# Performance work log

Measured on AMD Instinct MI355X. Metric: run time of the kernel, lower is better.

## Reference

```python
import jax, jax.numpy as jnp
import numpy as np

N_NODES = 50000


def gcn_conv(x, src, dst, deg_inv_sqrt, W, b, n_nodes):
    # GCNConv: h = x @ W; msg = norm * h[src]; out = scatter_add(msg, dst) + b
    h = x @ W  # [N, out]
    norm = deg_inv_sqrt[src] * deg_inv_sqrt[dst]  # symmetric normalization
    msg = h[src] * norm[:, None]  # [E+N, out]
    out = jax.ops.segment_sum(msg, dst, num_segments=n_nodes)
    return out + b


def setup_inputs() -> dict:
    key = jax.random.key(0)
    k_x, k_e, k_w1, k_w2 = jax.random.split(key, 4)
    in_c, hid, out_c = 256, 64, 64
    x = jax.random.normal(k_x, (N_NODES, 256), dtype=jnp.float32)
    edge_index = jax.random.randint(k_e, (2, 1600000), 0, N_NODES, dtype=jnp.int64)
    # Glorot-ish weights, zero bias as in GCNConv defaults
    W1 = jax.random.normal(k_w1, (in_c, hid), dtype=jnp.float32) / np.sqrt(in_c)
    b1 = jnp.zeros((hid,), dtype=jnp.float32)
    W2 = jax.random.normal(k_w2, (hid, out_c), dtype=jnp.float32) / np.sqrt(hid)
    b2 = jnp.zeros((out_c,), dtype=jnp.float32)
    return {"x": x, "edge_index": edge_index, "W1": W1, "b1": b1, "W2": W2, "b2": b2}


def reference(x, edge_index, W1, b1, W2, b2):
    n = x.shape[0]
    loops = jnp.arange(n, dtype=edge_index.dtype)
    src = jnp.concatenate([edge_index[0], loops])  # add self-loops
    dst = jnp.concatenate([edge_index[1], loops])
    deg = jax.ops.segment_sum(jnp.ones_like(dst, dtype=x.dtype), dst, num_segments=n)
    deg_inv_sqrt = jnp.where(deg > 0, jax.lax.rsqrt(deg), 0.0)
    h = gcn_conv(x, src, dst, deg_inv_sqrt, W1, b1, n)
    h = jax.nn.relu(h)
    out = gcn_conv(h, src, dst, deg_inv_sqrt, W2, b2, n)
    return out
```

## Files before the change

### kernel.cpp

```cpp
#include <hip/hip_runtime.h>
#include <hip/hip_bf16.h>


#define NB_MAX 1024

__device__ inline unsigned short f2bf(float f) {
    unsigned u = __builtin_bit_cast(unsigned, f);
    return (unsigned short)((u + 0x7FFFu + ((u >> 16) & 1u)) >> 16);
}
__device__ inline float blo(unsigned u) {
    return __builtin_bit_cast(float, u << 16);
}
__device__ inline float bhi(unsigned u) {
    return __builtin_bit_cast(float, u & 0xFFFF0000u);
}


__global__ __launch_bounds__(1024) void k_hist(const int* __restrict__ ei, int E,
                                               int nb, int chunk,
                                               int* __restrict__ histT) {
    __shared__ int h[NB_MAX];
    for (int i = threadIdx.x; i < nb; i += 1024) h[i] = 0;
    __syncthreads();
    int e0 = blockIdx.x * chunk, e1 = min(E, e0 + chunk);
    for (int e = e0 + threadIdx.x; e < e1; e += 1024)
        atomicAdd(&h[ei[E + e] >> 6], 1);
    __syncthreads();
    for (int b = threadIdx.x; b < nb; b += 1024)
        histT[b * 256 + blockIdx.x] = h[b];
}


__global__ __launch_bounds__(256) void k_scan_cols(int* __restrict__ histT,
                                                   int* __restrict__ total) {
    __shared__ int sm[256];
    int b = blockIdx.x, t = threadIdx.x;
    int v = histT[b * 256 + t];
    sm[t] = v;
    __syncthreads();
    for (int off = 1; off < 256; off <<= 1) {
        int u = (t >= off) ? sm[t - off] : 0;
        __syncthreads();
        sm[t] += u;
        __syncthreads();
    }
    histT[b * 256 + t] = sm[t] - v;
    if (t == 255) total[b] = sm[255];
}


__global__ __launch_bounds__(1024) void k_scan_totals(const int* __restrict__ total,
                                                      int* __restrict__ base, int nb) {
    __shared__ int sm[1024];
    int t = threadIdx.x;
    int v = (t < nb) ? total[t] : 0;
    sm[t] = v;
    __syncthreads();
    for (int off = 1; off < 1024; off <<= 1) {
        int u = (t >= off) ? sm[t - off] : 0;
        __syncthreads();
        sm[t] += u;
        __syncthreads();
    }
    if (t < nb) base[t] = sm[t] - v;
    if (t == nb - 1) base[nb] = sm[t];
}


__global__ __launch_bounds__(1024) void k_scatter(const int* __restrict__ ei, int E,
                                                  int nb, int chunk,
                                                  const int* __restrict__ histT,
                                                  const int* __restrict__ base,
                                                  unsigned* __restrict__ packed) {
    __shared__ int cur[NB_MAX];
    for (int b = threadIdx.x; b < nb; b += 1024)
        cur[b] = base[b] + histT[b * 256 + blockIdx.x];
    __syncthreads();
    int e0 = blockIdx.x * chunk, e1 = min(E, e0 + chunk);
    for (int e = e0 + threadIdx.x; e < e1; e += 1024) {
        int s = ei[e], d = ei[E + e];
        int pos = atomicAdd(&cur[d >> 6], 1);
        packed[pos] = (unsigned)s | ((unsigned)(d & 63) << 16);
    }
}


__global__ __launch_bounds__(1024) void k_csr(const unsigned* __restrict__ packed,
                                              const int* __restrict__ base,
                                              int n,
                                              int* __restrict__ qbeg,
                                              int* __restrict__ qcnt,
                                              float* __restrict__ dinv,
                                              unsigned short* __restrict__ ssrcp,
                                              unsigned short* __restrict__ hs1,
                                              unsigned short* __restrict__ hs2) {
    __shared__ int cnt[64];
    __shared__ int cur[64];
    const int b = blockIdx.x, t = threadIdx.x;
    const int p0 = base[b], p1 = base[b + 1];
    if (t < 64) cnt[t] = 0;
    __syncthreads();
    for (int p = p0 + t; p < p1; p += 1024)
        atomicAdd(&cnt[(packed[p] >> 16) & 63], 1);
    __syncthreads();
    if (t < 64) {
        int deg = cnt[t];
        int pdeg = (deg + 1) & ~1;
        int sum = pdeg;
#pragma unroll
        for (int d = 1; d < 64; d <<= 1) {
            int u = __shfl_up(sum, d, 64);
            if (t >= d) sum += u;
        }
        int excl = sum - pdeg;
        int pb = (2 + p0 + 128 * b + 1) & ~1;
        int start = pb + excl;
        int node = (b << 6) + t;
        if (node < n) {
            qbeg[node] = start >> 1;
            qcnt[node] = pdeg >> 1;
            dinv[node] = 1.0f / sqrtf((float)(deg + 1));
        }
        cur[t] = start;
    }
    __syncthreads();
    for (int p = p0 + t; p < p1; p += 1024) {
        unsigned k = packed[p];
        int pos = atomicAdd(&cur[(k >> 16) & 63], 1);
        ssrcp[pos] = (unsigned short)(k & 0xFFFFu);
    }
    __syncthreads();
    if (t < 64 && (cnt[t] & 1))
        ssrcp[cur[t]] = (unsigned short)n;
    if (b == 0) {
        if (t < 64) {
            hs1[(size_t)n * 64 + t] = 0;
            hs2[(size_t)n * 64 + t] = 0;
        }
        if (t == 0) {
            ssrcp[0] = (unsigned short)n;
            ssrcp[1] = (unsigned short)n;
        }
    }
}

#define FMA4(A, s, wv)                                                         \
    (A).x += (s) * (wv).x; (A).y += (s) * (wv).y;                              \
    (A).z += (s) * (wv).z; (A).w += (s) * (wv).w;


__global__ __launch_bounds__(256) void k_gemm256(const float* __restrict__ X,
                                                 const float* __restrict__ W,
                                                 const float* __restrict__ dinv,
                                                 unsigned short* __restrict__ HS,
                                                 int n) {
    const int K = 256;
    __shared__ float xl[128][36];
    __shared__ float wl[32][64];

    const int t = threadIdx.x;
    const int tc = t & 15;
    const int tr = t >> 4;
    const int row0 = blockIdx.x * 128;

    float4 acc[8];
#pragma unroll
    for (int r = 0; r < 8; ++r) acc[r] = make_float4(0.f, 0.f, 0.f, 0.f);

    for (int k0 = 0; k0 < K; k0 += 32) {
#pragma unroll
        for (int i = 0; i < 4; ++i) {
            int idx = i * 256 + t;
            int r = idx >> 3, f4 = idx & 7;
            int gr = row0 + r;
            float4 v = make_float4(0.f, 0.f, 0.f, 0.f);
            if (gr < n) v = *(const float4*)(X + (size_t)gr * K + k0 + f4 * 4);
            *(float4*)&xl[r][f4 * 4] = v;
        }
#pragma unroll
        for (int i = 0; i < 2; ++i) {
            int idx = i * 256 + t;
            int kr = idx >> 4, f4 = idx & 15;
            *(float4*)&wl[kr][f4 * 4] =
                *(const float4*)(W + (size_t)(k0 + kr) * 64 + f4 * 4);
        }
        __syncthreads();

#pragma unroll
        for (int kk = 0; kk < 32; kk += 4) {
            float4 wv0 = *(float4*)&wl[kk + 0][tc * 4];
            float4 wv1 = *(float4*)&wl[kk + 1][tc * 4];
            float4 wv2 = *(float4*)&wl[kk + 2][tc * 4];
            float4 wv3 = *(float4*)&wl[kk + 3][tc * 4];
#pragma unroll
            for (int r = 0; r < 8; ++r) {
                float4 xv = *(float4*)&xl[tr * 8 + r][kk];
                FMA4(acc[r], xv.x, wv0); FMA4(acc[r], xv.y, wv1);
                FMA4(acc[r], xv.z, wv2); FMA4(acc[r], xv.w, wv3);
            }
        }
        __syncthreads();
    }

#pragma unroll
    for (int r = 0; r < 8; ++r) {
        int gr = row0 + tr * 8 + r;
        if (gr < n) {
            float dv = dinv[gr];
            float4 o = acc[r];
            ushort4 pk;
            pk.x = f2bf(o.x * dv); pk.y = f2bf(o.y * dv);
            pk.z = f2bf(o.z * dv); pk.w = f2bf(o.w * dv);
            *(ushort4*)(HS + (size_t)gr * 64 + tc * 4) = pk;
        }
    }
}


template <int K>
__global__ __launch_bounds__(256) void k_gemm(const float* __restrict__ X,
                                              const float* __restrict__ W,
                                              const float* __restrict__ dinv,
                                              unsigned short* __restrict__ HS,
                                              int n) {
    __shared__ float xl[64][36];
    __shared__ float wl[32][64];

    const int t = threadIdx.x;
    const int tc = t & 15;
    const int tr = t >> 4;
    const int row0 = blockIdx.x * 64;

    float4 acc[4];
    acc[0] = acc[1] = acc[2] = acc[3] = make_float4(0.f, 0.f, 0.f, 0.f);

    for (int k0 = 0; k0 < K; k0 += 32) {
#pragma unroll
        for (int i = 0; i < 2; ++i) {
            int idx = i * 256 + t;
            int r = idx >> 3, f4 = idx & 7;
            int gr = row0 + r;
            float4 v = make_float4(0.f, 0.f, 0.f, 0.f);
            if (gr < n) v = *(const float4*)(X + (size_t)gr * K + k0 + f4 * 4);
            *(float4*)&xl[r][f4 * 4] = v;
        }
#pragma unroll
        for (int i = 0; i < 2; ++i) {
            int idx = i * 256 + t;
            int kr = idx >> 4, f4 = idx & 15;
            *(float4*)&wl[kr][f4 * 4] =
                *(const float4*)(W + (size_t)(k0 + kr) * 64 + f4 * 4);
        }
        __syncthreads();

#pragma unroll
        for (int kk = 0; kk < 32; kk += 4) {
            float4 xv0 = *(float4*)&xl[tr * 4 + 0][kk];
            float4 xv1 = *(float4*)&xl[tr * 4 + 1][kk];
            float4 xv2 = *(float4*)&xl[tr * 4 + 2][kk];
            float4 xv3 = *(float4*)&xl[tr * 4 + 3][kk];
            float4 wv0 = *(float4*)&wl[kk + 0][tc * 4];
            float4 wv1 = *(float4*)&wl[kk + 1][tc * 4];
            float4 wv2 = *(float4*)&wl[kk + 2][tc * 4];
            float4 wv3 = *(float4*)&wl[kk + 3][tc * 4];

            FMA4(acc[0], xv0.x, wv0); FMA4(acc[0], xv0.y, wv1);
            FMA4(acc[0], xv0.z, wv2); FMA4(acc[0], xv0.w, wv3);
            FMA4(acc[1], xv1.x, wv0); FMA4(acc[1], xv1.y, wv1);
            FMA4(acc[1], xv1.z, wv2); FMA4(acc[1], xv1.w, wv3);
            FMA4(acc[2], xv2.x, wv0); FMA4(acc[2], xv2.y, wv1);
            FMA4(acc[2], xv2.z, wv2); FMA4(acc[2], xv2.w, wv3);
            FMA4(acc[3], xv3.x, wv0); FMA4(acc[3], xv3.y, wv1);
            FMA4(acc[3], xv3.z, wv2); FMA4(acc[3], xv3.w, wv3);
        }
        __syncthreads();
    }

#pragma unroll
    for (int ri = 0; ri < 4; ++ri) {
        int gr = row0 + tr * 4 + ri;
        if (gr < n) {
            float dv = dinv[gr];
            float4 o = acc[ri];
            ushort4 pk;
            pk.x = f2bf(o.x * dv); pk.y = f2bf(o.y * dv);
            pk.z = f2bf(o.z * dv); pk.w = f2bf(o.w * dv);
            *(ushort4*)(HS + (size_t)gr * 64 + tc * 4) = pk;
        }
    }
}


template <bool RELU>
__global__ __launch_bounds__(256) void k_agg(const unsigned short* __restrict__ hs,
                      const int* __restrict__ qbeg,
                      const int* __restrict__ qcnt,
                      const unsigned short* __restrict__ ssrcp,
                      const float* __restrict__ dinv,
                      const float* __restrict__ bias,
                      float* __restrict__ out, int n) {
    int node = blockIdx.x * 4 + (threadIdx.x >> 6);
    if (node >= n) return;
    node = __builtin_amdgcn_readfirstlane(node);
    const int lane = threadIdx.x & 63;
    const int c = lane & 7;
    const int shH = (lane & 8) ? 16 : 0;

    const uint4* hs4 = (const uint4*)hs;
    const unsigned* ssu = (const unsigned*)ssrcp;

    const int q0 = qbeg[node];
    const int m  = qcnt[node];

    const uint4 sv = hs4[(size_t)node * 8 + c];
    const float dv = dinv[node];
    const float4 bv0 = *(const float4*)(bias + 8 * c);
    const float4 bv1 = *(const float4*)(bias + 8 * c + 4);

    float ax[8];
#pragma unroll
    for (int k = 0; k < 8; ++k) ax[k] = 0.f;

    int qb = 0;
    for (; qb + 8 <= m; qb += 8) {
        unsigned ssl[8];
#pragma unroll
        for (int j = 0; j < 8; ++j) ssl[j] = ssu[q0 + qb + j];
        uint4 v[2];
#pragma unroll
        for (int i = 0; i < 2; ++i) {
            unsigned w = (lane & 32) ? ((lane & 16) ? ssl[4 * i + 3] : ssl[4 * i + 2])
                                     : ((lane & 16) ? ssl[4 * i + 1] : ssl[4 * i + 0]);
            int s = (int)((w >> shH) & 0xFFFFu);
            v[i] = hs4[(size_t)s * 8 + c];
        }
#pragma unroll
        for (int i = 0; i < 2; ++i) {
            ax[0] += blo(v[i].x); ax[1] += bhi(v[i].x);
            ax[2] += blo(v[i].y); ax[3] += bhi(v[i].y);
            ax[4] += blo(v[i].z); ax[5] += bhi(v[i].z);
            ax[6] += blo(v[i].w); ax[7] += bhi(v[i].w);
        }
    }
    const int rem = m - qb;
    if (rem) {
        unsigned ssl[8];
#pragma unroll
        for (int j = 0; j < 8; ++j) {
            int q = (j < rem) ? (q0 + qb + j) : 0;
            ssl[j] = ssu[q];
        }
        uint4 v[2];
#pragma unroll
        for (int i = 0; i < 2; ++i) {
            unsigned w = (lane & 32) ? ((lane & 16) ? ssl[4 * i + 3] : ssl[4 * i + 2])
                                     : ((lane & 16) ? ssl[4 * i + 1] : ssl[4 * i + 0]);
            int s = (int)((w >> shH) & 0xFFFFu);
            v[i] = hs4[(size_t)s * 8 + c];
        }
#pragma unroll
        for (int i = 0; i < 2; ++i) {
            ax[0] += blo(v[i].x); ax[1] += bhi(v[i].x);
            ax[2] += blo(v[i].y); ax[3] += bhi(v[i].y);
            ax[4] += blo(v[i].z); ax[5] += bhi(v[i].z);
            ax[6] += blo(v[i].w); ax[7] += bhi(v[i].w);
        }
    }

#pragma unroll
    for (int k = 0; k < 8; ++k) {
        ax[k] += __shfl_xor(ax[k], 8, 64);
        ax[k] += __shfl_xor(ax[k], 16, 64);
        ax[k] += __shfl_xor(ax[k], 32, 64);
    }

    float r[8];
    r[0] = dv * (ax[0] + blo(sv.x)) + bv0.x;
    r[1] = dv * (ax[1] + bhi(sv.x)) + bv0.y;
    r[2] = dv * (ax[2] + blo(sv.y)) + bv0.z;
    r[3] = dv * (ax[3] + bhi(sv.y)) + bv0.w;
    r[4] = dv * (ax[4] + blo(sv.z)) + bv1.x;
    r[5] = dv * (ax[5] + bhi(sv.z)) + bv1.y;
    r[6] = dv * (ax[6] + blo(sv.w)) + bv1.z;
    r[7] = dv * (ax[7] + bhi(sv.w)) + bv1.w;
    if (RELU) {
#pragma unroll
        for (int k = 0; k < 8; ++k) r[k] = fmaxf(r[k], 0.f);
    }
    if (lane < 16) {
        float4 o = (lane & 8) ? make_float4(r[4], r[5], r[6], r[7])
                              : make_float4(r[0], r[1], r[2], r[3]);
        *(float4*)(out + (size_t)node * 64 + 8 * c + 4 * ((lane >> 3) & 1)) = o;
    }
}


extern "C" void kernel_launch(void* const* d_in, const int* in_sizes, int n_in,
                              void* d_out, int out_size, void* d_ws, size_t ws_size,
                              hipStream_t stream) {
    const float* x  = (const float*)d_in[0];
    const int*   ei = (const int*)d_in[1];
    const float* W1 = (const float*)d_in[2];
    const float* b1 = (const float*)d_in[3];
    const float* W2 = (const float*)d_in[4];
    const float* b2 = (const float*)d_in[5];

    const int n = in_sizes[0] / 256;
    const int E = in_sizes[1] / 2;
    const int nb = (n + 63) >> 6;
    const int chunk = (E + 255) / 256;

    char* ws = (char*)d_ws;
    auto carve = [&](size_t bytes) {
        void* p = (void*)ws;
        ws += (bytes + 255) & ~(size_t)255;
        return p;
    };
    int*            histT  = (int*)carve((size_t)nb * 256 * 4);
    int*            total  = (int*)carve((size_t)nb * 4);
    int*            base   = (int*)carve((size_t)(nb + 1) * 4);
    unsigned*       packed = (unsigned*)carve((size_t)E * 4);
    unsigned short* ssrcp  = (unsigned short*)carve(((size_t)E + 128 * nb + 256) * 2);
    int*            qbeg   = (int*)carve((size_t)n * 4);
    int*            qcnt   = (int*)carve((size_t)n * 4);
    float*          dinv   = (float*)carve((size_t)n * 4);
    unsigned short* hs1    = (unsigned short*)carve((size_t)(n + 1) * 64 * 2);
    float*          hB     = (float*)carve((size_t)n * 64 * 4);
    unsigned short* hs2    = (unsigned short*)carve((size_t)(n + 1) * 64 * 2);

    k_hist<<<256, 1024, 0, stream>>>(ei, E, nb, chunk, histT);
    k_scan_cols<<<nb, 256, 0, stream>>>(histT, total);
    k_scan_totals<<<1, 1024, 0, stream>>>(total, base, nb);
    k_scatter<<<256, 1024, 0, stream>>>(ei, E, nb, chunk, histT, base, packed);
    k_csr<<<nb, 1024, 0, stream>>>(packed, base, n, qbeg, qcnt, dinv, ssrcp,
                                   hs1, hs2);

    const int nbG1 = (n + 127) / 128;
    const int nbG2 = (n + 63) / 64;
    const int nbA  = (n + 3) / 4;

    k_gemm256<<<nbG1, 256, 0, stream>>>(x, W1, dinv, hs1, n);
    k_agg<true><<<nbA, 256, 0, stream>>>(hs1, qbeg, qcnt, ssrcp, dinv,
                                         b1, hB, n);

    k_gemm<64><<<nbG2, 256, 0, stream>>>(hB, W2, dinv, hs2, n);
    k_agg<false><<<nbA, 256, 0, stream>>>(hs2, qbeg, qcnt, ssrcp, dinv,
                                          b2, (float*)d_out, n);
}
```

Measured before the change: 225.2 us.

## Split first-layer GEMM along K into two partial passes plus a finalize kernel

The 256-wide first GEMM now runs as a split-K kernel. Each of two grid slices computes a 128-deep partial product over 64-row tiles and writes it in fp32. A new finalize kernel sums the two partials, applies the degree scaling and packs the result to bf16. This is meant to raise the block count and occupancy of the first GEMM, at the cost of an extra launch and roughly 25 MB of extra fp32 write and read traffic.

New measurement: 221.6 us. Within noise of the previous version (-1.6%).

```diff
diff --git a/kernel.cpp b/kernel.cpp
--- a/kernel.cpp
+++ b/kernel.cpp
@@ -149,27 +149,28 @@
     (A).z += (s) * (wv).z; (A).w += (s) * (wv).w;
 
 
-__global__ __launch_bounds__(256) void k_gemm256(const float* __restrict__ X,
-                                                 const float* __restrict__ W,
-                                                 const float* __restrict__ dinv,
-                                                 unsigned short* __restrict__ HS,
-                                                 int n) {
+__global__ __launch_bounds__(256) void k_gemm256s(const float* __restrict__ X,
+                                                  const float* __restrict__ W,
+                                                  float* __restrict__ hsF0,
+                                                  float* __restrict__ hsF1,
+                                                  int n) {
     const int K = 256;
-    __shared__ float xl[128][36];
+    __shared__ float xl[64][36];
     __shared__ float wl[32][64];
 
     const int t = threadIdx.x;
     const int tc = t & 15;
     const int tr = t >> 4;
-    const int row0 = blockIdx.x * 128;
-
-    float4 acc[8];
-#pragma unroll
-    for (int r = 0; r < 8; ++r) acc[r] = make_float4(0.f, 0.f, 0.f, 0.f);
-
-    for (int k0 = 0; k0 < K; k0 += 32) {
-#pragma unroll
-        for (int i = 0; i < 4; ++i) {
+    const int row0 = blockIdx.x * 64;
+    const int ky = blockIdx.y;
+    float* __restrict__ dst = ky ? hsF1 : hsF0;
+
+    float4 acc[4];
+    acc[0] = acc[1] = acc[2] = acc[3] = make_float4(0.f, 0.f, 0.f, 0.f);
+
+    for (int k0 = ky * 128; k0 < ky * 128 + 128; k0 += 32) {
+#pragma unroll
+        for (int i = 0; i < 2; ++i) {
             int idx = i * 256 + t;
             int r = idx >> 3, f4 = idx & 7;
             int gr = row0 + r;
@@ -188,32 +189,52 @@
 
 #pragma unroll
         for (int kk = 0; kk < 32; kk += 4) {
+            float4 xv0 = *(float4*)&xl[tr * 4 + 0][kk];
+            float4 xv1 = *(float4*)&xl[tr * 4 + 1][kk];
+            float4 xv2 = *(float4*)&xl[tr * 4 + 2][kk];
+            float4 xv3 = *(float4*)&xl[tr * 4 + 3][kk];
             float4 wv0 = *(float4*)&wl[kk + 0][tc * 4];
             float4 wv1 = *(float4*)&wl[kk + 1][tc * 4];
             float4 wv2 = *(float4*)&wl[kk + 2][tc * 4];
             float4 wv3 = *(float4*)&wl[kk + 3][tc * 4];
-#pragma unroll
-            for (int r = 0; r < 8; ++r) {
-                float4 xv = *(float4*)&xl[tr * 8 + r][kk];
-                FMA4(acc[r], xv.x, wv0); FMA4(acc[r], xv.y, wv1);
-                FMA4(acc[r], xv.z, wv2); FMA4(acc[r], xv.w, wv3);
-            }
-        }
-        __syncthreads();
-    }
-
-#pragma unroll
-    for (int r = 0; r < 8; ++r) {
-        int gr = row0 + tr * 8 + r;
-        if (gr < n) {
-            float dv = dinv[gr];
-            float4 o = acc[r];
-            ushort4 pk;
-            pk.x = f2bf(o.x * dv); pk.y = f2bf(o.y * dv);
-            pk.z = f2bf(o.z * dv); pk.w = f2bf(o.w * dv);
-            *(ushort4*)(HS + (size_t)gr * 64 + tc * 4) = pk;
-        }
-    }
+
+            FMA4(acc[0], xv0.x, wv0); FMA4(acc[0], xv0.y, wv1);
+            FMA4(acc[0], xv0.z, wv2); FMA4(acc[0], xv0.w, wv3);
+            FMA4(acc[1], xv1.x, wv0); FMA4(acc[1], xv1.y, wv1);
+            FMA4(acc[1], xv1.z, wv2); FMA4(acc[1], xv1.w, wv3);
+            FMA4(acc[2], xv2.x, wv0); FMA4(acc[2], xv2.y, wv1);
+            FMA4(acc[2], xv2.z, wv2); FMA4(acc[2], xv2.w, wv3);
+            FMA4(acc[3], xv3.x, wv0); FMA4(acc[3], xv3.y, wv1);
+            FMA4(acc[3], xv3.z, wv2); FMA4(acc[3], xv3.w, wv3);
+        }
+        __syncthreads();
+    }
+
+#pragma unroll
+    for (int ri = 0; ri < 4; ++ri) {
+        int gr = row0 + tr * 4 + ri;
+        if (gr < n)
+            *(float4*)(dst + (size_t)gr * 64 + tc * 4) = acc[ri];
+    }
+}
+
+
+__global__ __launch_bounds__(1024) void k_fin(const float* __restrict__ hsF0,
+                                              const float* __restrict__ hsF1,
+                                              const float* __restrict__ dinv,
+                                              unsigned short* __restrict__ HS,
+                                              int n) {
+    int i = blockIdx.x * 1024 + threadIdx.x;
+    if (i >= n * 16) return;
+    float4 a = *(const float4*)(hsF0 + (size_t)i * 4);
+    float4 b = *(const float4*)(hsF1 + (size_t)i * 4);
+    float dv = dinv[i >> 4];
+    ushort4 pk;
+    pk.x = f2bf((a.x + b.x) * dv);
+    pk.y = f2bf((a.y + b.y) * dv);
+    pk.z = f2bf((a.z + b.z) * dv);
+    pk.w = f2bf((a.w + b.w) * dv);
+    *(ushort4*)(HS + (size_t)i * 4) = pk;
 }
 
 
@@ -427,6 +448,7 @@
     unsigned short* hs1    = (unsigned short*)carve((size_t)(n + 1) * 64 * 2);
     float*          hB     = (float*)carve((size_t)n * 64 * 4);
     unsigned short* hs2    = (unsigned short*)carve((size_t)(n + 1) * 64 * 2);
+    float*          hsF1   = (float*)carve((size_t)n * 64 * 4);
 
     k_hist<<<256, 1024, 0, stream>>>(ei, E, nb, chunk, histT);
     k_scan_cols<<<nb, 256, 0, stream>>>(histT, total);
@@ -435,15 +457,16 @@
     k_csr<<<nb, 1024, 0, stream>>>(packed, base, n, qbeg, qcnt, dinv, ssrcp,
                                    hs1, hs2);
 
-    const int nbG1 = (n + 127) / 128;
-    const int nbG2 = (n + 63) / 64;
-    const int nbA  = (n + 3) / 4;
-
-    k_gemm256<<<nbG1, 256, 0, stream>>>(x, W1, dinv, hs1, n);
+    const int nbG = (n + 63) / 64;
+    const int nbA = (n + 3) / 4;
+    const int nbF = (n * 16 + 1023) / 1024;
+
+    k_gemm256s<<<dim3(nbG, 2), 256, 0, stream>>>(x, W1, hB, hsF1, n);
+    k_fin<<<nbF, 1024, 0, stream>>>(hB, hsF1, dinv, hs1, n);
     k_agg<true><<<nbA, 256, 0, stream>>>(hs1, qbeg, qcnt, ssrcp, dinv,
                                          b1, hB, n);
 
-    k_gemm<64><<<nbG2, 256, 0, stream>>>(hB, W2, dinv, hs2, n);
+    k_gemm<64><<<nbG, 256, 0, stream>>>(hB, W2, dinv, hs2, n);
     k_agg<false><<<nbA, 256, 0, stream>>>(hs2, qbeg, qcnt, ssrcp, dinv,
                                           b2, (float*)d_out, n);
 }
```
